# Kernel optimization log

Hardware: AMD Instinct MI355X
Metric: run time of the kernel (lower is better)

The kernel has to match this reference:

```python
import jax, jax.numpy as jnp
import numpy as np

N_NODES = 50000
N_EDGES = 1600000
N_GRAPHS = 128
IN_C, HID, N_CLS = 128, 256, 10


def setup_inputs() -> dict:
    key = jax.random.key(0)
    ks = jax.random.split(key, 8)
    x = jax.random.normal(ks[0], (N_NODES, IN_C), dtype=jnp.float32)
    edge_index = jax.random.randint(ks[1], (2, N_EDGES), 0, N_NODES, dtype=jnp.int64)
    batch = jnp.sort(jax.random.randint(ks[2], (N_NODES,), 0, N_GRAPHS, dtype=jnp.int64))
    def glorot(k, shape):
        lim = np.sqrt(6.0 / (shape[0] + shape[1]))
        return jax.random.uniform(k, shape, jnp.float32, -lim, lim)
    return {
        "x": x, "edge_index": edge_index, "batch": batch,
        "W1": glorot(ks[3], (IN_C, HID)), "b1": jnp.zeros((HID,), jnp.float32),
        "W2": glorot(ks[4], (HID, HID)), "b2": jnp.zeros((HID,), jnp.float32),
        "Wl1": glorot(ks[5], (HID, 64)), "bl1": jnp.zeros((64,), jnp.float32),
        "Wl2": glorot(ks[6], (64, N_CLS)), "bl2": jnp.zeros((N_CLS,), jnp.float32),
    }


def _gcn_conv(x, row, col, deg_inv_sqrt, W, b):
    h = x @ W                                  # [N, out]
    norm = deg_inv_sqrt[row] * deg_inv_sqrt[col]   # [E]
    msg = h[row] * norm[:, None]                   # gather + scale
    agg = jax.ops.segment_sum(msg, col, num_segments=x.shape[0])
    agg = agg + h * (deg_inv_sqrt * deg_inv_sqrt)[:, None]  # self-loop term (norm = 1/deg)
    return agg + b


def reference(x, edge_index, batch, W1, b1, W2, b2, Wl1, bl1, Wl2, bl2):
    N = x.shape[0]
    row, col = edge_index[0], edge_index[1]
    # degree including self-loop, computed on target nodes (PyG convention)
    deg = jax.ops.segment_sum(jnp.ones((row.shape[0],), x.dtype), col, num_segments=N) + 1.0
    deg_inv_sqrt = jax.lax.rsqrt(deg)

    h = jax.nn.relu(_gcn_conv(x, row, col, deg_inv_sqrt, W1, b1))
    h = jax.nn.relu(_gcn_conv(h, row, col, deg_inv_sqrt, W2, b2))

    # global_mean_pool over batch ids
    sums = jax.ops.segment_sum(h, batch, num_segments=N_GRAPHS)
    cnts = jax.ops.segment_sum(jnp.ones((N,), h.dtype), batch, num_segments=N_GRAPHS)
    g = sums / jnp.maximum(cnts, 1.0)[:, None]     # [G, HID]

    g = jax.nn.relu(g @ Wl1 + bl1)
    return jax.nn.log_softmax(g @ Wl2 + bl2, axis=1)
```

## Files before the change

kernel.cpp:

```cpp
#include <hip/hip_runtime.h>
#include <hip/hip_bf16.h>
#include <math.h>

#define NN 50000
#define NG 128
#define INC 128
#define HIDC 256
#define NCLS 10

#define NBLK 256
#define BSH 8
#define NB 196

typedef _Float16 h8_t __attribute__((ext_vector_type(8)));
typedef _Float16 h2_t __attribute__((ext_vector_type(2)));
typedef __attribute__((ext_vector_type(4))) float f4_t;

__device__ inline f4_t mfma16(h8_t a, h8_t b, f4_t c) {
  return __builtin_amdgcn_mfma_f32_16x16x32_f16(a, b, c, 0, 0, 0);
}

__device__ inline ushort f2h(float f) {
  _Float16 h = (_Float16)f; return *(ushort*)&h;
}
__device__ inline float h2f(ushort u) {
  _Float16 h = *(_Float16*)&u; return (float)h;
}

union U2 { uint2 u; struct { h2_t x, y; } h; };
union UW { unsigned u; h2_t h; };

__device__ inline void gload_lds16(const void* g, void* l) {
  __builtin_amdgcn_global_load_lds(
      (const __attribute__((address_space(1))) unsigned int*)g,
      (__attribute__((address_space(3))) unsigned int*)l, 16, 0, 0);
}

__device__ inline int lbound(const int* __restrict__ a, int n, int key) {
  int lo = 0, hi = n;
  while (lo < hi) { int m = (lo + hi) >> 1; if (a[m] < key) lo = m + 1; else hi = m; }
  return lo;
}

__global__ __launch_bounds__(256) void edge_hist(const int* __restrict__ ecol,
                                                 int* __restrict__ hist, int E, int chunk) {
  __shared__ int h[NB];
  int blk = blockIdx.x;
  for (int i = threadIdx.x; i < NB; i += 256) h[i] = 0;
  __syncthreads();
  int e0 = blk * chunk, e1 = min(e0 + chunk, E);
  for (int e = e0 + threadIdx.x; e < e1; e += 256)
    atomicAdd(&h[ecol[e] >> BSH], 1);
  __syncthreads();
  for (int i = threadIdx.x; i < NB; i += 256) hist[i * NBLK + blk] = h[i];
}

__global__ __launch_bounds__(256) void edge_partition(const int* __restrict__ erow,
                                                      const int* __restrict__ ecol,
                                                      const int* __restrict__ histBase,
                                                      unsigned* __restrict__ part,
                                                      int E, int chunk) {
  __shared__ int cur[NB];
  int blk = blockIdx.x;
  for (int i = threadIdx.x; i < NB; i += 256) cur[i] = histBase[i * NBLK + blk];
  __syncthreads();
  int e0 = blk * chunk, e1 = min(e0 + chunk, E);
  for (int e = e0 + threadIdx.x; e < e1; e += 256) {
    int c = ecol[e];
    int b = c >> BSH;
    int pos = atomicAdd(&cur[b], 1);
    part[pos] = ((unsigned)erow[e] << 8) | (unsigned)(c & 255);
  }
}

__global__ __launch_bounds__(256) void bucket_off_dis(const unsigned* __restrict__ part,
                                                      const int* __restrict__ histBase,
                                                      int* __restrict__ offsets,
                                                      float* __restrict__ dis, int N) {
  __shared__ int cnt[256];
  __shared__ int sm[256];
  int b = blockIdx.x, t = threadIdx.x;
  cnt[t] = 0;
  __syncthreads();
  int s0 = histBase[b * NBLK];
  int s1 = histBase[(b + 1) * NBLK];
  for (int e = s0 + t; e < s1; e += 256)
    atomicAdd(&cnt[part[e] & 255], 1);
  __syncthreads();
  int v = cnt[t];
  sm[t] = v;
  __syncthreads();
  #pragma unroll
  for (int off = 1; off < 256; off <<= 1) {
    int x = (t >= off) ? sm[t - off] : 0;
    __syncthreads();
    sm[t] += x;
    __syncthreads();
  }
  int excl = (t == 0) ? 0 : sm[t - 1];
  int node = (b << BSH) + t;
  if (node < N) {
    offsets[node] = s0 + excl;
    dis[node] = rsqrtf((float)v + 1.0f);
  } else if (node == N) {
    offsets[N] = s0 + excl;
  }
}

__global__ __launch_bounds__(256) void bucket_csr_ew(const unsigned* __restrict__ part,
                                                     const int* __restrict__ histBase,
                                                     const int* __restrict__ offsets,
                                                     const float* __restrict__ dis,
                                                     unsigned* __restrict__ ew, int N) {
  __shared__ int cur[256];
  __shared__ float sdis[256];
  int b = blockIdx.x;
  int node = (b << BSH) + threadIdx.x;
  cur[threadIdx.x] = (node < N) ? offsets[node] : 0;
  sdis[threadIdx.x] = (node < N) ? dis[node] : 0.0f;
  __syncthreads();
  int s0 = histBase[b * NBLK];
  int s1 = histBase[(b + 1) * NBLK];
  for (int e = s0 + threadIdx.x; e < s1; e += 256) {
    unsigned pv = part[e];
    int c = pv & 255;
    int r = (int)(pv >> 8);
    int pos = atomicAdd(&cur[c], 1);
    float w = dis[r] * sdis[c];
    ew[pos] = ((unsigned)r << 16) | (unsigned)f2h(w);
  }
}

#define SCAN_T 256
#define SCAN_V 8
#define SCAN_VPB (SCAN_T * SCAN_V)

__global__ __launch_bounds__(SCAN_T) void scanA(const int* __restrict__ deg,
                                                int* __restrict__ offsets,
                                                int* __restrict__ blockTotals, int n) {
  __shared__ int sm[SCAN_T];
  int b = blockIdx.x;
  int t = threadIdx.x;
  int base = b * SCAN_VPB + t * SCAN_V;
  int v[SCAN_V];
  int run = 0;
  #pragma unroll
  for (int j = 0; j < SCAN_V; ++j) {
    int idx = base + j;
    int d = (idx < n) ? deg[idx] : 0;
    run += d;
    v[j] = run;
  }
  sm[t] = run;
  __syncthreads();
  #pragma unroll
  for (int off = 1; off < SCAN_T; off <<= 1) {
    int x = (t >= off) ? sm[t - off] : 0;
    __syncthreads();
    sm[t] += x;
    __syncthreads();
  }
  int excl = (t == 0) ? 0 : sm[t - 1];
  #pragma unroll
  for (int j = 0; j < SCAN_V; ++j) {
    int idx = base + j;
    if (idx < n) offsets[idx + 1] = v[j] + excl;
  }
  if (t == SCAN_T - 1) blockTotals[b] = sm[t];
}

__global__ void scanB(int* __restrict__ blockTotals, int nb) {
  if (threadIdx.x == 0 && blockIdx.x == 0) {
    int run = 0;
    for (int i = 0; i < nb; ++i) {
      int v = blockTotals[i];
      blockTotals[i] = run;
      run += v;
    }
  }
}

__global__ void scanC(int* __restrict__ offsets, const int* __restrict__ blockTotals, int n) {
  int stride = gridDim.x * blockDim.x;
  for (int i = blockIdx.x * blockDim.x + threadIdx.x; i < n; i += stride) {
    offsets[i + 1] += blockTotals[i / SCAN_VPB];
    if (i == 0) offsets[0] = 0;
  }
}

__global__ void cast_all(const float* __restrict__ x, unsigned* __restrict__ xcb,
                         const float* __restrict__ W1, ushort* __restrict__ W1T,
                         const float* __restrict__ W2, ushort* __restrict__ W2T, int N) {
  int idx = blockIdx.x * 256 + threadIdx.x;
  int nx = N * 64;
  if (idx < nx) {
    int n = idx >> 6, pp = idx & 63;
    float v0 = x[(long)n * 128 + 2 * pp];
    float v1 = x[(long)n * 128 + 2 * pp + 1];
    xcb[((long)(pp >> 4) * N + n) * 16 + (pp & 15)] =
        (unsigned)f2h(v0) | ((unsigned)f2h(v1) << 16);
    return;
  }
  int i1 = idx - nx;
  if (i1 < INC * HIDC) {
    int k = i1 / HIDC, n = i1 % HIDC;
    W1T[(long)n * INC + k] = f2h(W1[i1]);
    return;
  }
  int i2 = i1 - INC * HIDC;
  if (i2 < HIDC * HIDC) {
    int k = i2 / HIDC, n = i2 % HIDC;
    W2T[(long)n * HIDC + k] = f2h(W2[i2]);
  }
}

template <int MODE>
__global__ __launch_bounds__(256) void aggregate_cb(
    const uint2* __restrict__ xcb, const float* __restrict__ dis,
    const int* __restrict__ offsets, const unsigned* __restrict__ ew,
    uint2* __restrict__ outcb, int N) {
  int blk = blockIdx.x;
  int slice, nb;
  if (MODE == 0) { slice = blk & 7; nb = blk >> 3; }
  else           { slice = (blk >> 1) & 3; nb = ((blk >> 3) << 1) | (blk & 1); }
  int node = nb * 32 + (threadIdx.x >> 3);
  if (node >= N) return;
  int cl = threadIdx.x & 7;
  const uint2* xs = xcb + (long)slice * N * 8;
  uint2* os = outcb + (long)slice * N * 8;
  float di = dis[node];
  _Float16 ddh = (_Float16)(di * di);
  h2_t dd2 = {ddh, ddh};
  U2 sv; sv.u = xs[node * 8 + cl];
  h2_t ax = sv.h.x * dd2, ay = sv.h.y * dd2;
  h2_t bx = {0, 0}, by = {0, 0};
  h2_t cx = {0, 0}, cy = {0, 0};
  h2_t dx = {0, 0}, dy = {0, 0};
  int e = offsets[node], eE = offsets[node + 1];
  for (; e + 7 < eE; e += 8) {
    unsigned p0 = ew[e],     p1 = ew[e + 1], p2 = ew[e + 2], p3 = ew[e + 3];
    unsigned p4 = ew[e + 4], p5 = ew[e + 5], p6 = ew[e + 6], p7 = ew[e + 7];
    U2 v0, v1, v2, v3, v4, v5, v6, v7;
    v0.u = xs[(p0 >> 16) * 8 + cl];
    v1.u = xs[(p1 >> 16) * 8 + cl];
    v2.u = xs[(p2 >> 16) * 8 + cl];
    v3.u = xs[(p3 >> 16) * 8 + cl];
    v4.u = xs[(p4 >> 16) * 8 + cl];
    v5.u = xs[(p5 >> 16) * 8 + cl];
    v6.u = xs[(p6 >> 16) * 8 + cl];
    v7.u = xs[(p7 >> 16) * 8 + cl];
    UW q0, q1, q2, q3, q4, q5, q6, q7;
    q0.u = p0; q1.u = p1; q2.u = p2; q3.u = p3;
    q4.u = p4; q5.u = p5; q6.u = p6; q7.u = p7;
    h2_t w0 = {q0.h[0], q0.h[0]}, w1 = {q1.h[0], q1.h[0]};
    h2_t w2 = {q2.h[0], q2.h[0]}, w3 = {q3.h[0], q3.h[0]};
    h2_t w4 = {q4.h[0], q4.h[0]}, w5 = {q5.h[0], q5.h[0]};
    h2_t w6 = {q6.h[0], q6.h[0]}, w7 = {q7.h[0], q7.h[0]};
    ax = v0.h.x * w0 + ax; ay = v0.h.y * w0 + ay;
    bx = v1.h.x * w1 + bx; by = v1.h.y * w1 + by;
    cx = v2.h.x * w2 + cx; cy = v2.h.y * w2 + cy;
    dx = v3.h.x * w3 + dx; dy = v3.h.y * w3 + dy;
    ax = v4.h.x * w4 + ax; ay = v4.h.y * w4 + ay;
    bx = v5.h.x * w5 + bx; by = v5.h.y * w5 + by;
    cx = v6.h.x * w6 + cx; cy = v6.h.y * w6 + cy;
    dx = v7.h.x * w7 + dx; dy = v7.h.y * w7 + dy;
  }
  for (; e < eE; ++e) {
    unsigned p0 = ew[e];
    U2 v0; v0.u = xs[(p0 >> 16) * 8 + cl];
    UW q0; q0.u = p0;
    h2_t w0 = {q0.h[0], q0.h[0]};
    ax = v0.h.x * w0 + ax; ay = v0.h.y * w0 + ay;
  }
  ax = ax + bx + cx + dx;
  ay = ay + by + cy + dy;
  U2 o; o.h.x = ax; o.h.y = ay;
  os[node * 8 + cl] = o.u;
}

template <int K, bool OUTCB>
__global__ __launch_bounds__(256) void gemm_mfma(
    const ushort* __restrict__ A, const ushort* __restrict__ WT,
    const float* __restrict__ bias, ushort* __restrict__ outb, int M) {
  __shared__ ushort smem[16384];
  const int tid = threadIdx.x;
  const int lane = tid & 63;
  const int wave = tid >> 6;
  const int wm = wave >> 1, wn = wave & 1;
  const int m0 = blockIdx.x * 128;
  const int n0 = blockIdx.y * 128;

  f4_t acc[4][4] = {};

  for (int k0 = 0; k0 < K; k0 += 64) {
    __syncthreads();
    #pragma unroll
    for (int is = 0; is < 4; ++is) {
      int s = is * 256 + tid;
      int row = s >> 3;
      int ch = (s & 7) ^ (row & 7);
      int k = k0 + ch * 8;
      long grow = m0 + row; if (grow > M - 1) grow = M - 1;
      const ushort* g = A + ((long)(k >> 5) * M + grow) * 32 + (k & 31);
      gload_lds16(g, &smem[(is * 256 + wave * 64) * 8]);
    }
    #pragma unroll
    for (int is = 0; is < 4; ++is) {
      int s = is * 256 + tid;
      int row = s >> 3;
      int ch = (s & 7) ^ (row & 7);
      const ushort* g = WT + (long)(n0 + row) * K + k0 + ch * 8;
      gload_lds16(g, &smem[8192 + (is * 256 + wave * 64) * 8]);
    }
    asm volatile("s_waitcnt vmcnt(0)" ::: "memory");
    __syncthreads();
    #pragma unroll
    for (int ks = 0; ks < 2; ++ks) {
      h8_t af[4], bfr[4];
      #pragma unroll
      for (int mi = 0; mi < 4; ++mi) {
        int row = wm * 64 + mi * 16 + (lane & 15);
        int ch = (ks * 4 + (lane >> 4)) ^ (row & 7);
        af[mi] = *(const h8_t*)(&smem[row * 64 + ch * 8]);
      }
      #pragma unroll
      for (int ni = 0; ni < 4; ++ni) {
        int row = wn * 64 + ni * 16 + (lane & 15);
        int ch = (ks * 4 + (lane >> 4)) ^ (row & 7);
        bfr[ni] = *(const h8_t*)(&smem[8192 + row * 64 + ch * 8]);
      }
      #pragma unroll
      for (int mi = 0; mi < 4; ++mi)
        #pragma unroll
        for (int ni = 0; ni < 4; ++ni)
          acc[mi][ni] = mfma16(af[mi], bfr[ni], acc[mi][ni]);
    }
  }
  #pragma unroll
  for (int ni = 0; ni < 4; ++ni) {
    int col = n0 + wn * 64 + ni * 16 + (lane & 15);
    float bb = bias[col];
    #pragma unroll
    for (int mi = 0; mi < 4; ++mi) {
      #pragma unroll
      for (int r = 0; r < 4; ++r) {
        int row = m0 + wm * 64 + mi * 16 + (lane >> 4) * 4 + r;
        if (row < M) {
          float v = fmaxf(acc[mi][ni][r] + bb, 0.0f);
          if (OUTCB)
            outb[((long)(col >> 5) * M + row) * 32 + (col & 31)] = f2h(v);
          else
            outb[(long)row * HIDC + col] = f2h(v);
        }
      }
    }
  }
}

#define POOL_SPLIT 8
__global__ __launch_bounds__(HIDC) void pool_range_f16(const ushort* __restrict__ h,
                                                       const int* __restrict__ batch,
                                                       float* __restrict__ gsum, int N) {
  int g = blockIdx.x;
  int s = blockIdx.y;
  int c = threadIdx.x;
  int s0 = lbound(batch, N, g);
  int s1 = lbound(batch, N, g + 1);
  int len = s1 - s0;
  int chunk = (len + POOL_SPLIT - 1) / POOL_SPLIT;
  int i0 = s0 + s * chunk;
  int i1 = min(i0 + chunk, s1);
  float acc = 0.0f;
  for (int i = i0; i < i1; ++i) acc += h2f(h[(long)i * HIDC + c]);
  if (i1 > i0) atomicAdd(&gsum[g * HIDC + c], acc);
}

__global__ __launch_bounds__(64) void mlp_kernel(
    const float* __restrict__ gsum, const int* __restrict__ batch,
    const float* __restrict__ Wl1, const float* __restrict__ bl1,
    const float* __restrict__ Wl2, const float* __restrict__ bl2,
    float* __restrict__ out, int N) {
  __shared__ float g[HIDC];
  __shared__ float hid[64];
  __shared__ float logits[NCLS];
  __shared__ float red[2];
  int i = blockIdx.x;
  int t = threadIdx.x;
  int cnt = lbound(batch, N, i + 1) - lbound(batch, N, i);
  float inv = 1.0f / fmaxf((float)cnt, 1.0f);
  for (int c = t; c < HIDC; c += 64) g[c] = gsum[i * HIDC + c] * inv;
  __syncthreads();
  float acc = bl1[t];
  for (int c = 0; c < HIDC; ++c) acc = fmaf(g[c], Wl1[c * 64 + t], acc);
  hid[t] = fmaxf(acc, 0.0f);
  __syncthreads();
  if (t < NCLS) {
    float l = bl2[t];
    for (int c = 0; c < 64; ++c) l = fmaf(hid[c], Wl2[c * NCLS + t], l);
    logits[t] = l;
  }
  __syncthreads();
  if (t == 0) {
    float m = -1e30f;
    for (int k = 0; k < NCLS; ++k) m = fmaxf(m, logits[k]);
    float s = 0.f;
    for (int k = 0; k < NCLS; ++k) s += expf(logits[k] - m);
    red[0] = m;
    red[1] = logf(s);
  }
  __syncthreads();
  if (t < NCLS) out[i * NCLS + t] = logits[t] - red[0] - red[1];
}

extern "C" void kernel_launch(void* const* d_in, const int* in_sizes, int n_in,
                              void* d_out, int out_size, void* d_ws, size_t ws_size,
                              hipStream_t stream) {
  const float* x = (const float*)d_in[0];
  const int* edge_index = (const int*)d_in[1];
  const int* batch = (const int*)d_in[2];
  const float* W1 = (const float*)d_in[3];
  const float* b1 = (const float*)d_in[4];
  const float* W2 = (const float*)d_in[5];
  const float* b2 = (const float*)d_in[6];
  const float* Wl1 = (const float*)d_in[7];
  const float* bl1 = (const float*)d_in[8];
  const float* Wl2 = (const float*)d_in[9];
  const float* bl2 = (const float*)d_in[10];
  float* out = (float*)d_out;

  const int N = in_sizes[0] / INC;
  const int E = in_sizes[1] / 2;
  const int* erow = edge_index;
  const int* ecol = edge_index + E;

  char* p = (char*)d_ws;
  auto alloc = [&](size_t bytes) {
    void* r = (void*)p;
    p += (bytes + 255) & ~(size_t)255;
    return r;
  };
  float* dis = (float*)alloc((size_t)N * 4);
  int* offsets = (int*)alloc((size_t)(N + 1) * 4);
  unsigned* ew = (unsigned*)alloc((size_t)E * 4);
  unsigned* part = (unsigned*)alloc((size_t)E * 4);
  int* hist = (int*)alloc((size_t)(NB * NBLK) * 4);
  int* histBase = (int*)alloc((size_t)(NB * NBLK + 1) * 4);
  float* gsum = (float*)alloc((size_t)NG * HIDC * 4);
  int* blockTotals = (int*)alloc((size_t)256 * 4);
  ushort* W1T = (ushort*)alloc((size_t)INC * HIDC * 2);
  ushort* W2T = (ushort*)alloc((size_t)HIDC * HIDC * 2);
  unsigned* x_cb = (unsigned*)alloc((size_t)N * INC * 2);
  unsigned* agg1_cb = (unsigned*)alloc((size_t)N * INC * 2);
  unsigned* h1_cb = (unsigned*)alloc((size_t)N * HIDC * 2);
  unsigned* agg2_cb = (unsigned*)alloc((size_t)N * HIDC * 2);
  ushort* h2 = (ushort*)x_cb;

  hipMemsetAsync(gsum, 0, (size_t)NG * HIDC * 4, stream);

  const int chunk = (E + NBLK - 1) / NBLK;
  edge_hist<<<NBLK, 256, 0, stream>>>(ecol, hist, E, chunk);
  {
    const int nh = NB * NBLK;
    const int nbh = (nh + SCAN_VPB - 1) / SCAN_VPB;
    scanA<<<nbh, SCAN_T, 0, stream>>>(hist, histBase, blockTotals, nh);
    scanB<<<1, 64, 0, stream>>>(blockTotals, nbh);
    scanC<<<(nh + 255) / 256, 256, 0, stream>>>(histBase, blockTotals, nh);
  }
  edge_partition<<<NBLK, 256, 0, stream>>>(erow, ecol, histBase, part, E, chunk);
  bucket_off_dis<<<NB, 256, 0, stream>>>(part, histBase, offsets, dis, N);
  bucket_csr_ew<<<NB, 256, 0, stream>>>(part, histBase, offsets, dis, ew, N);

  {
    int tot = N * 64 + INC * HIDC + HIDC * HIDC;
    cast_all<<<(tot + 255) / 256, 256, 0, stream>>>(x, x_cb, W1, W1T, W2, W2T, N);
  }

  {
    const int nb2 = (N + 63) / 64;
    aggregate_cb<1><<<nb2 << 3, 256, 0, stream>>>(
        (const uint2*)x_cb, dis, offsets, ew, (uint2*)agg1_cb, N);
  }
  {
    dim3 grid((N + 127) / 128, HIDC / 128);
    gemm_mfma<INC, true><<<grid, 256, 0, stream>>>(
        (const ushort*)agg1_cb, W1T, b1, (ushort*)h1_cb, N);
  }
  {
    const int nodeblks = (N + 31) / 32;
    aggregate_cb<0><<<nodeblks << 3, 256, 0, stream>>>(
        (const uint2*)h1_cb, dis, offsets, ew, (uint2*)agg2_cb, N);
  }
  {
    dim3 grid((N + 127) / 128, HIDC / 128);
    gemm_mfma<HIDC, false><<<grid, 256, 0, stream>>>(
        (const ushort*)agg2_cb, W2T, b2, h2, N);
  }
  {
    dim3 pgrid(NG, POOL_SPLIT);
    pool_range_f16<<<pgrid, HIDC, 0, stream>>>(h2, batch, gsum, N);
  }
  mlp_kernel<<<NG, 64, 0, stream>>>(gsum, batch, Wl1, bl1, Wl2, bl2, out, N);
}
```

Measured before the change: 396.8 us.

## Pad CSR rows to multiples of 8 for vector edge loads; drop pool atomics

Each node's CSR segment in the edge-weight array now starts on a multiple-of-8 boundary, and a separate end array records the true degree. This lets the aggregation loop fetch eight packed edge entries with two 128-bit loads instead of eight scalar loads. Building it takes a split count kernel, a single-thread scan over the padded bucket totals, and a bucket kernel that recomputes the padded prefix. Pooling now writes per-split partial sums that the MLP kernel reduces, which removes the memset and the float atomics. The cost is two extra small launches and a larger edge array.

Measured after the change: 403.2 us. Within noise of the previous version (+1.6%).

```diff
diff --git a/kernel.cpp b/kernel.cpp
--- a/kernel.cpp
+++ b/kernel.cpp
@@ -73,10 +73,11 @@
   }
 }
 
-__global__ __launch_bounds__(256) void bucket_off_dis(const unsigned* __restrict__ part,
-                                                      const int* __restrict__ histBase,
-                                                      int* __restrict__ offsets,
-                                                      float* __restrict__ dis, int N) {
+__global__ __launch_bounds__(256) void bucket_cnt(const unsigned* __restrict__ part,
+                                                  const int* __restrict__ histBase,
+                                                  int* __restrict__ deg,
+                                                  float* __restrict__ dis,
+                                                  int* __restrict__ padTot, int N) {
   __shared__ int cnt[256];
   __shared__ int sm[256];
   int b = blockIdx.x, t = threadIdx.x;
@@ -88,7 +89,8 @@
     atomicAdd(&cnt[part[e] & 255], 1);
   __syncthreads();
   int v = cnt[t];
-  sm[t] = v;
+  int pc = (v + 7) & ~7;
+  sm[t] = pc;
   __syncthreads();
   #pragma unroll
   for (int off = 1; off < 256; off <<= 1) {
@@ -97,31 +99,57 @@
     sm[t] += x;
     __syncthreads();
   }
-  int excl = (t == 0) ? 0 : sm[t - 1];
   int node = (b << BSH) + t;
   if (node < N) {
-    offsets[node] = s0 + excl;
+    deg[node] = v;
     dis[node] = rsqrtf((float)v + 1.0f);
-  } else if (node == N) {
-    offsets[N] = s0 + excl;
-  }
-}
-
-__global__ __launch_bounds__(256) void bucket_csr_ew(const unsigned* __restrict__ part,
-                                                     const int* __restrict__ histBase,
-                                                     const int* __restrict__ offsets,
-                                                     const float* __restrict__ dis,
-                                                     unsigned* __restrict__ ew, int N) {
+  }
+  if (t == 255) padTot[b] = sm[255];
+}
+
+__global__ void padscan(int* __restrict__ padTot, int* __restrict__ padBase, int nb) {
+  if (threadIdx.x == 0 && blockIdx.x == 0) {
+    int run = 0;
+    for (int i = 0; i < nb; ++i) { padBase[i] = run; run += padTot[i]; }
+  }
+}
+
+__global__ __launch_bounds__(256) void bucket_ew(const unsigned* __restrict__ part,
+                                                 const int* __restrict__ histBase,
+                                                 const int* __restrict__ padBase,
+                                                 const int* __restrict__ deg,
+                                                 const float* __restrict__ dis,
+                                                 int* __restrict__ offsets,
+                                                 int* __restrict__ dend,
+                                                 unsigned* __restrict__ ew, int N) {
   __shared__ int cur[256];
+  __shared__ int sm[256];
   __shared__ float sdis[256];
-  int b = blockIdx.x;
-  int node = (b << BSH) + threadIdx.x;
-  cur[threadIdx.x] = (node < N) ? offsets[node] : 0;
-  sdis[threadIdx.x] = (node < N) ? dis[node] : 0.0f;
+  int b = blockIdx.x, t = threadIdx.x;
+  int node = (b << BSH) + t;
+  int v = (node < N) ? deg[node] : 0;
+  int pc = (v + 7) & ~7;
+  sm[t] = pc;
+  sdis[t] = (node < N) ? dis[node] : 0.0f;
+  __syncthreads();
+  #pragma unroll
+  for (int off = 1; off < 256; off <<= 1) {
+    int x = (t >= off) ? sm[t - off] : 0;
+    __syncthreads();
+    sm[t] += x;
+    __syncthreads();
+  }
+  int excl = (t == 0) ? 0 : sm[t - 1];
+  int obase = padBase[b] + excl;
+  cur[t] = obase;
+  if (node < N) {
+    offsets[node] = obase;
+    dend[node] = obase + v;
+  }
   __syncthreads();
   int s0 = histBase[b * NBLK];
   int s1 = histBase[(b + 1) * NBLK];
-  for (int e = s0 + threadIdx.x; e < s1; e += 256) {
+  for (int e = s0 + t; e < s1; e += 256) {
     unsigned pv = part[e];
     int c = pv & 255;
     int r = (int)(pv >> 8);
@@ -217,8 +245,8 @@
 template <int MODE>
 __global__ __launch_bounds__(256) void aggregate_cb(
     const uint2* __restrict__ xcb, const float* __restrict__ dis,
-    const int* __restrict__ offsets, const unsigned* __restrict__ ew,
-    uint2* __restrict__ outcb, int N) {
+    const int* __restrict__ offsets, const int* __restrict__ dend,
+    const unsigned* __restrict__ ew, uint2* __restrict__ outcb, int N) {
   int blk = blockIdx.x;
   int slice, nb;
   if (MODE == 0) { slice = blk & 7; nb = blk >> 3; }
@@ -236,22 +264,22 @@
   h2_t bx = {0, 0}, by = {0, 0};
   h2_t cx = {0, 0}, cy = {0, 0};
   h2_t dx = {0, 0}, dy = {0, 0};
-  int e = offsets[node], eE = offsets[node + 1];
+  int e = offsets[node], eE = dend[node];
   for (; e + 7 < eE; e += 8) {
-    unsigned p0 = ew[e],     p1 = ew[e + 1], p2 = ew[e + 2], p3 = ew[e + 3];
-    unsigned p4 = ew[e + 4], p5 = ew[e + 5], p6 = ew[e + 6], p7 = ew[e + 7];
+    uint4 pa = *(const uint4*)(ew + e);
+    uint4 pb = *(const uint4*)(ew + e + 4);
     U2 v0, v1, v2, v3, v4, v5, v6, v7;
-    v0.u = xs[(p0 >> 16) * 8 + cl];
-    v1.u = xs[(p1 >> 16) * 8 + cl];
-    v2.u = xs[(p2 >> 16) * 8 + cl];
-    v3.u = xs[(p3 >> 16) * 8 + cl];
-    v4.u = xs[(p4 >> 16) * 8 + cl];
-    v5.u = xs[(p5 >> 16) * 8 + cl];
-    v6.u = xs[(p6 >> 16) * 8 + cl];
-    v7.u = xs[(p7 >> 16) * 8 + cl];
+    v0.u = xs[(pa.x >> 16) * 8 + cl];
+    v1.u = xs[(pa.y >> 16) * 8 + cl];
+    v2.u = xs[(pa.z >> 16) * 8 + cl];
+    v3.u = xs[(pa.w >> 16) * 8 + cl];
+    v4.u = xs[(pb.x >> 16) * 8 + cl];
+    v5.u = xs[(pb.y >> 16) * 8 + cl];
+    v6.u = xs[(pb.z >> 16) * 8 + cl];
+    v7.u = xs[(pb.w >> 16) * 8 + cl];
     UW q0, q1, q2, q3, q4, q5, q6, q7;
-    q0.u = p0; q1.u = p1; q2.u = p2; q3.u = p3;
-    q4.u = p4; q5.u = p5; q6.u = p6; q7.u = p7;
+    q0.u = pa.x; q1.u = pa.y; q2.u = pa.z; q3.u = pa.w;
+    q4.u = pb.x; q5.u = pb.y; q6.u = pb.z; q7.u = pb.w;
     h2_t w0 = {q0.h[0], q0.h[0]}, w1 = {q1.h[0], q1.h[0]};
     h2_t w2 = {q2.h[0], q2.h[0]}, w3 = {q3.h[0], q3.h[0]};
     h2_t w4 = {q4.h[0], q4.h[0]}, w5 = {q5.h[0], q5.h[0]};
@@ -358,25 +386,28 @@
 }
 
 #define POOL_SPLIT 8
-__global__ __launch_bounds__(HIDC) void pool_range_f16(const ushort* __restrict__ h,
-                                                       const int* __restrict__ batch,
-                                                       float* __restrict__ gsum, int N) {
+__global__ __launch_bounds__(HIDC) void pool_partial(const ushort* __restrict__ h,
+                                                     const int* __restrict__ batch,
+                                                     float* __restrict__ psum, int N) {
+  __shared__ int bounds[2];
   int g = blockIdx.x;
   int s = blockIdx.y;
   int c = threadIdx.x;
-  int s0 = lbound(batch, N, g);
-  int s1 = lbound(batch, N, g + 1);
+  if (c == 0) bounds[0] = lbound(batch, N, g);
+  if (c == 1) bounds[1] = lbound(batch, N, g + 1);
+  __syncthreads();
+  int s0 = bounds[0], s1 = bounds[1];
   int len = s1 - s0;
   int chunk = (len + POOL_SPLIT - 1) / POOL_SPLIT;
   int i0 = s0 + s * chunk;
   int i1 = min(i0 + chunk, s1);
   float acc = 0.0f;
   for (int i = i0; i < i1; ++i) acc += h2f(h[(long)i * HIDC + c]);
-  if (i1 > i0) atomicAdd(&gsum[g * HIDC + c], acc);
+  psum[((long)g * POOL_SPLIT + s) * HIDC + c] = acc;
 }
 
 __global__ __launch_bounds__(64) void mlp_kernel(
-    const float* __restrict__ gsum, const int* __restrict__ batch,
+    const float* __restrict__ psum, const int* __restrict__ batch,
     const float* __restrict__ Wl1, const float* __restrict__ bl1,
     const float* __restrict__ Wl2, const float* __restrict__ bl2,
     float* __restrict__ out, int N) {
@@ -388,7 +419,13 @@
   int t = threadIdx.x;
   int cnt = lbound(batch, N, i + 1) - lbound(batch, N, i);
   float inv = 1.0f / fmaxf((float)cnt, 1.0f);
-  for (int c = t; c < HIDC; c += 64) g[c] = gsum[i * HIDC + c] * inv;
+  for (int c = t; c < HIDC; c += 64) {
+    float s = 0.0f;
+    #pragma unroll
+    for (int k = 0; k < POOL_SPLIT; ++k)
+      s += psum[((long)i * POOL_SPLIT + k) * HIDC + c];
+    g[c] = s * inv;
+  }
   __syncthreads();
   float acc = bl1[t];
   for (int c = 0; c < HIDC; ++c) acc = fmaf(g[c], Wl1[c * 64 + t], acc);
@@ -440,12 +477,16 @@
     return r;
   };
   float* dis = (float*)alloc((size_t)N * 4);
+  int* deg = (int*)alloc((size_t)N * 4);
   int* offsets = (int*)alloc((size_t)(N + 1) * 4);
-  unsigned* ew = (unsigned*)alloc((size_t)E * 4);
+  int* dend = (int*)alloc((size_t)N * 4);
+  unsigned* ew = (unsigned*)alloc(((size_t)E + 8 * (size_t)N) * 4);
   unsigned* part = (unsigned*)alloc((size_t)E * 4);
   int* hist = (int*)alloc((size_t)(NB * NBLK) * 4);
   int* histBase = (int*)alloc((size_t)(NB * NBLK + 1) * 4);
-  float* gsum = (float*)alloc((size_t)NG * HIDC * 4);
+  int* padTot = (int*)alloc((size_t)NB * 4);
+  int* padBase = (int*)alloc((size_t)NB * 4);
+  float* psum = (float*)alloc((size_t)NG * POOL_SPLIT * HIDC * 4);
   int* blockTotals = (int*)alloc((size_t)256 * 4);
   ushort* W1T = (ushort*)alloc((size_t)INC * HIDC * 2);
   ushort* W2T = (ushort*)alloc((size_t)HIDC * HIDC * 2);
@@ -455,8 +496,6 @@
   unsigned* agg2_cb = (unsigned*)alloc((size_t)N * HIDC * 2);
   ushort* h2 = (ushort*)x_cb;
 
-  hipMemsetAsync(gsum, 0, (size_t)NG * HIDC * 4, stream);
-
   const int chunk = (E + NBLK - 1) / NBLK;
   edge_hist<<<NBLK, 256, 0, stream>>>(ecol, hist, E, chunk);
   {
@@ -467,8 +506,10 @@
     scanC<<<(nh + 255) / 256, 256, 0, stream>>>(histBase, blockTotals, nh);
   }
   edge_partition<<<NBLK, 256, 0, stream>>>(erow, ecol, histBase, part, E, chunk);
-  bucket_off_dis<<<NB, 256, 0, stream>>>(part, histBase, offsets, dis, N);
-  bucket_csr_ew<<<NB, 256, 0, stream>>>(part, histBase, offsets, dis, ew, N);
+  bucket_cnt<<<NB, 256, 0, stream>>>(part, histBase, deg, dis, padTot, N);
+  padscan<<<1, 64, 0, stream>>>(padTot, padBase, NB);
+  bucket_ew<<<NB, 256, 0, stream>>>(part, histBase, padBase, deg, dis,
+                                    offsets, dend, ew, N);
 
   {
     int tot = N * 64 + INC * HIDC + HIDC * HIDC;
@@ -478,7 +519,7 @@
   {
     const int nb2 = (N + 63) / 64;
     aggregate_cb<1><<<nb2 << 3, 256, 0, stream>>>(
-        (const uint2*)x_cb, dis, offsets, ew, (uint2*)agg1_cb, N);
+        (const uint2*)x_cb, dis, offsets, dend, ew, (uint2*)agg1_cb, N);
   }
   {
     dim3 grid((N + 127) / 128, HIDC / 128);
@@ -488,7 +529,7 @@
   {
     const int nodeblks = (N + 31) / 32;
     aggregate_cb<0><<<nodeblks << 3, 256, 0, stream>>>(
-        (const uint2*)h1_cb, dis, offsets, ew, (uint2*)agg2_cb, N);
+        (const uint2*)h1_cb, dis, offsets, dend, ew, (uint2*)agg2_cb, N);
   }
   {
     dim3 grid((N + 127) / 128, HIDC / 128);
@@ -497,7 +538,7 @@
   }
   {
     dim3 pgrid(NG, POOL_SPLIT);
-    pool_range_f16<<<pgrid, HIDC, 0, stream>>>(h2, batch, gsum, N);
-  }
-  mlp_kernel<<<NG, 64, 0, stream>>>(gsum, batch, Wl1, bl1, Wl2, bl2, out, N);
-}
+    pool_partial<<<pgrid, HIDC, 0, stream>>>(h2, batch, psum, N);
+  }
+  mlp_kernel<<<NG, 64, 0, stream>>>(psum, batch, Wl1, bl1, Wl2, bl2, out, N);
+}
```
